# Kernel tuning notes

Measured on AMD Instinct MI355X. Metric: run time of the kernel, lower is better.

Reference implementation:

```python
import jax, jax.numpy as jnp
import numpy as np

EPS = 1e-5
TOP_K = 2


def setup_inputs() -> dict:
    key = jax.random.key(0)
    ks = jax.random.split(key, 8)
    B, T, D, E, F = 4, 2048, 1024, 8, 4096
    s_in = 1.0 / np.sqrt(D)
    s_ff = 1.0 / np.sqrt(F)
    return {
        "hidden_states": jax.random.normal(ks[0], (B, T, D), jnp.float32),
        "input_tensor": jax.random.normal(ks[1], (B, T, D), jnp.float32),
        "gate_w": jax.random.normal(ks[2], (D, E), jnp.float32) * s_in,
        "gate_b": jnp.zeros((E,), jnp.float32),
        "w1": jax.random.normal(ks[3], (E, D, F), jnp.float32) * s_in,
        "b1": jnp.zeros((E, F), jnp.float32),
        "w2": jax.random.normal(ks[4], (E, F, D), jnp.float32) * s_ff,
        "b2": jnp.zeros((E, D), jnp.float32),
        "gamma": jnp.ones((D,), jnp.float32),
        "beta": jnp.zeros((D,), jnp.float32),
    }


def _layer_norm(x, gamma, beta):
    mu = jnp.mean(x, axis=-1, keepdims=True)
    var = jnp.mean(jnp.square(x - mu), axis=-1, keepdims=True)
    return (x - mu) * jax.lax.rsqrt(var + EPS) * gamma + beta


def reference(hidden_states, input_tensor, gate_w, gate_b, w1, b1, w2, b2, gamma, beta):
    E = gate_b.shape[0]
    # Router: softmax over experts, then top-k gate values/indices.
    gate_logits = jnp.einsum("btd,de->bte", hidden_states, gate_w) + gate_b
    gate_probs = jax.nn.softmax(gate_logits, axis=-1)
    topk_gates, topk_idx = jax.lax.top_k(gate_probs, TOP_K)  # [B,T,K]
    # Combine weights per expert: sum of top-k gate values routed to expert e.
    combine_w = jnp.sum(
        jax.nn.one_hot(topk_idx, E, dtype=hidden_states.dtype)
        * topk_gates[..., None],
        axis=-2,
    )  # [B,T,E]
    # Dispatch/combine: weighted sum of expert FFN outputs (loop over small fixed E).
    expert_outputs = jnp.zeros_like(hidden_states)
    for e in range(E):
        h = jax.nn.gelu(jnp.einsum("btd,df->btf", hidden_states, w1[e]) + b1[e])
        y = jnp.einsum("btf,fd->btd", h, w2[e]) + b2[e]
        expert_outputs = expert_outputs + combine_w[..., e:e + 1] * y
    # Dropout is identity in eval mode.
    return _layer_norm(expert_outputs + input_tensor, gamma, beta)
```

## Files before the change

kernel.cpp:

```cpp
#include <hip/hip_runtime.h>

#define TOKENS 8192
#define DIM 1024
#define NEXP 8
#define FDIM 4096

typedef __bf16 bf16x8 __attribute__((ext_vector_type(8)));
typedef float f32x4 __attribute__((ext_vector_type(4)));
typedef float f32x16 __attribute__((ext_vector_type(16)));

__device__ __forceinline__ unsigned short f2bf(float f) {
  unsigned u = __builtin_bit_cast(unsigned, f);
  u += 0x7fffu + ((u >> 16) & 1u);
  return (unsigned short)(u >> 16);
}

__device__ __forceinline__ float bf2f(unsigned short s) {
  unsigned u = (unsigned)s << 16;
  return __builtin_bit_cast(float, u);
}

__device__ __forceinline__ void gload16(const void* g, void* l) {
  __builtin_amdgcn_global_load_lds(
      (const __attribute__((address_space(1))) unsigned int*)g,
      (__attribute__((address_space(3))) unsigned int*)l, 16, 0, 0);
}

__global__ void zero_counts_kernel(int* counts) {
  if (threadIdx.x < NEXP) counts[threadIdx.x] = 0;
}

__global__ void scan_kernel(const int* counts, int* offs, int* nchk,
                            int* chunks0, int* chunks1) {
  if (threadIdx.x == 0) {
    int s = 0;
    for (int e = 0; e < NEXP; ++e) { offs[e] = s; s += counts[e]; }
    offs[NEXP] = s;
    int nc0 = 0, nc1 = 0;
    for (int e = 0; e < NEXP; ++e) {
      const int mt = (counts[e] + 127) >> 7;
      for (int mc = 0; mc < mt; mc += 4) {
        for (int n4 = 0; n4 < 32; n4 += 4)
          chunks0[nc0++] = (e << 16) | (mc << 8) | n4;
        for (int n4 = 0; n4 < 8; n4 += 4)
          chunks1[nc1++] = (e << 16) | (mc << 8) | n4;
      }
    }
    nchk[0] = nc0;
    nchk[1] = nc1;
  }
}

__global__ void router_kernel(const float* __restrict__ hs,
                              const float* __restrict__ gw,
                              const float* __restrict__ gb,
                              int* __restrict__ counts,
                              int* __restrict__ tok_idx,
                              float* __restrict__ tok_w,
                              unsigned int* __restrict__ slotinfo,
                              unsigned short* __restrict__ hs_bf) {
  const int lane = threadIdx.x & 63;
  const int wid = threadIdx.x >> 6;
  const int t = blockIdx.x * 4 + wid;
  const float* row = hs + (size_t)t * DIM;

  float x[16];
  const float4* r4 = (const float4*)(row + lane * 16);
#pragma unroll
  for (int i = 0; i < 4; ++i) {
    float4 v = r4[i];
    x[i * 4 + 0] = v.x; x[i * 4 + 1] = v.y; x[i * 4 + 2] = v.z; x[i * 4 + 3] = v.w;
  }

  float acc[8];
#pragma unroll
  for (int e = 0; e < 8; ++e) acc[e] = 0.f;
#pragma unroll
  for (int i = 0; i < 16; ++i) {
    const int d = lane * 16 + i;
    const float4* g4 = (const float4*)(gw + (size_t)d * 8);
    float4 g0 = g4[0], g1 = g4[1];
    const float xv = x[i];
    acc[0] += xv * g0.x; acc[1] += xv * g0.y; acc[2] += xv * g0.z; acc[3] += xv * g0.w;
    acc[4] += xv * g1.x; acc[5] += xv * g1.y; acc[6] += xv * g1.z; acc[7] += xv * g1.w;
  }
#pragma unroll
  for (int sh = 1; sh < 64; sh <<= 1) {
#pragma unroll
    for (int e = 0; e < 8; ++e) acc[e] += __shfl_xor(acc[e], sh, 64);
  }
#pragma unroll
  for (int e = 0; e < 8; ++e) acc[e] += gb[e];

  float mx = acc[0];
#pragma unroll
  for (int e = 1; e < 8; ++e) mx = fmaxf(mx, acc[e]);
  float p[8];
  float sum = 0.f;
#pragma unroll
  for (int e = 0; e < 8; ++e) { p[e] = __expf(acc[e] - mx); sum += p[e]; }
  const float inv = 1.0f / sum;

  int i0 = 0; float b0 = p[0];
#pragma unroll
  for (int e = 1; e < 8; ++e) if (p[e] > b0) { b0 = p[e]; i0 = e; }
  int i1 = -1; float b1v = -1.f;
#pragma unroll
  for (int e = 0; e < 8; ++e) if (e != i0 && p[e] > b1v) { b1v = p[e]; i1 = e; }

  if (lane == 0) {
    int pos0 = atomicAdd(&counts[i0], 1);
    tok_idx[i0 * TOKENS + pos0] = t;
    tok_w[i0 * TOKENS + pos0] = b0 * inv;
    int pos1 = atomicAdd(&counts[i1], 1);
    tok_idx[i1 * TOKENS + pos1] = t;
    tok_w[i1 * TOKENS + pos1] = b1v * inv;
    slotinfo[t] = ((unsigned)i0 << 29) | ((unsigned)pos0 << 16) |
                  ((unsigned)i1 << 13) | (unsigned)pos1;
  }

  unsigned short us[16];
#pragma unroll
  for (int i = 0; i < 16; ++i) us[i] = f2bf(x[i]);
  uint4 o0, o1;
  o0.x = (unsigned)us[0] | ((unsigned)us[1] << 16);
  o0.y = (unsigned)us[2] | ((unsigned)us[3] << 16);
  o0.z = (unsigned)us[4] | ((unsigned)us[5] << 16);
  o0.w = (unsigned)us[6] | ((unsigned)us[7] << 16);
  o1.x = (unsigned)us[8] | ((unsigned)us[9] << 16);
  o1.y = (unsigned)us[10] | ((unsigned)us[11] << 16);
  o1.z = (unsigned)us[12] | ((unsigned)us[13] << 16);
  o1.w = (unsigned)us[14] | ((unsigned)us[15] << 16);
  uint4* dst = (uint4*)(hs_bf + (size_t)t * DIM + lane * 16);
  dst[0] = o0;
  dst[1] = o1;
}

__global__ void cast_transpose_all(const float* __restrict__ w1,
                                   unsigned short* __restrict__ w1t,
                                   const float* __restrict__ w2,
                                   unsigned short* __restrict__ w2t) {
  __shared__ float tile[64][65];
  const int L = blockIdx.x;
  const float* src;
  unsigned short* dstp;
  int R, C, bi;
  if (L < 8192) { src = w1; dstp = w1t; R = DIM;  C = FDIM; bi = L; }
  else          { src = w2; dstp = w2t; R = FDIM; C = DIM;  bi = L - 8192; }
  const int nx = C >> 6;
  const int e = bi >> 10;
  const int w = bi & 1023;
  const int by = w / nx, bx = w % nx;
  const int r0 = by * 64, c0 = bx * 64;
  const float* s = src + (size_t)e * R * C;
  unsigned int* d = (unsigned int*)(dstp + (size_t)e * R * C);

#pragma unroll
  for (int i = 0; i < 16; ++i) {
    const int idx = threadIdx.x + i * 256;
    const int r = idx >> 6;
    const int c = idx & 63;
    tile[r][c] = s[(size_t)(r0 + r) * C + (c0 + c)];
  }
  __syncthreads();
#pragma unroll
  for (int i = 0; i < 8; ++i) {
    const int idx = threadIdx.x + i * 256;
    const int c = idx >> 5;
    const int r = (idx & 31) * 2;
    unsigned pk = (unsigned)f2bf(tile[r][c]) | ((unsigned)f2bf(tile[r + 1][c]) << 16);
    d[((size_t)(c0 + c) * R + (r0 + r)) >> 1] = pk;
  }
}

template<int MODE, int K, int N>
__global__ __launch_bounds__(256, 4)
void moe_gemm(const unsigned short* __restrict__ Abase,
              const unsigned short* __restrict__ Bbase,
              const float* __restrict__ bias,
              const int* __restrict__ counts,
              const int* __restrict__ offs,
              const int* __restrict__ tok_idx,
              const int* __restrict__ chunktab,
              const int* __restrict__ nchk,
              unsigned short* __restrict__ dst) {
  constexpr int NS = K / 32;
  __shared__ __align__(16) unsigned char sm[32768];

  const int L = blockIdx.x;
  const int xk = L & 7;
  const int tt = L >> 3;
  const int g = (tt >> 4) * 8 + xk;
  if (g >= nchk[MODE]) return;
  const int within = tt & 15;
  const int cd = chunktab[g];
  const int e = cd >> 16;
  const int cnt = counts[e];
  const int m0 = (((cd >> 8) & 255) + (within >> 2)) * 128;
  if (m0 >= cnt) return;
  const int n0 = ((cd & 255) + (within & 3)) * 128;
  const int goff = offs[e];

  const int tid = threadIdx.x;
  const int lane = tid & 63;
  const int wid = tid >> 6;
  const int wm = wid >> 1;
  const int wn = wid & 1;
  const int l31 = lane & 31;
  const int lh = lane >> 5;

  const int trow = tid >> 2;
  const int tswz = (tid & 3) ^ ((trow >> 1) & 3);
  const unsigned char* Bexp = (const unsigned char*)(Bbase + (size_t)e * K * N);

  int gA0 = m0 + trow;      if (gA0 > cnt - 1) gA0 = cnt - 1;
  int gA1 = m0 + trow + 64; if (gA1 > cnt - 1) gA1 = cnt - 1;
  size_t rowA0, rowA1;
  if (MODE == 0) {
    rowA0 = (size_t)tok_idx[e * TOKENS + gA0] * K;
    rowA1 = (size_t)tok_idx[e * TOKENS + gA1] * K;
  } else {
    rowA0 = (size_t)(goff + gA0) * K;
    rowA1 = (size_t)(goff + gA1) * K;
  }
  const unsigned char* pA0 = (const unsigned char*)(Abase + rowA0) + tswz * 16;
  const unsigned char* pA1 = (const unsigned char*)(Abase + rowA1) + tswz * 16;
  const unsigned char* pB0 = Bexp + (size_t)(n0 + trow) * (K * 2) + tswz * 16;
  const unsigned char* pB1 = Bexp + (size_t)(n0 + trow + 64) * (K * 2) + tswz * 16;

  const int sw = (l31 >> 1) & 3;
  const int cE = lh ^ sw;
  const int aB = wm * 4096 + l31 * 64 + cE * 16;
  const int bB = 8192 + wn * 4096 + l31 * 64 + cE * 16;
  const unsigned char* smc = (const unsigned char*)sm;
  unsigned char* smw = (unsigned char*)sm + tid * 16;

  f32x16 acc[2][2];
#pragma unroll
  for (int mb = 0; mb < 2; ++mb)
#pragma unroll
    for (int nb = 0; nb < 2; ++nb)
#pragma unroll
      for (int r = 0; r < 16; ++r) acc[mb][nb][r] = 0.f;

  gload16(pA0, smw);
  gload16(pA1, smw + 4096);
  gload16(pB0, smw + 8192);
  gload16(pB1, smw + 12288);
  pA0 += 64; pA1 += 64; pB0 += 64; pB1 += 64;

#pragma unroll 1
  for (int st = 0; st < NS; ++st) {
    const int cs = (st & 1) << 14;
    const int ns = ((st + 1) & 1) << 14;
    if (st < NS - 1) {
      gload16(pA0, smw + ns);
      gload16(pA1, smw + ns + 4096);
      gload16(pB0, smw + ns + 8192);
      gload16(pB1, smw + ns + 12288);
      pA0 += 64; pA1 += 64; pB0 += 64; pB1 += 64;
      asm volatile("s_waitcnt vmcnt(4)" ::: "memory");
    } else {
      asm volatile("s_waitcnt vmcnt(0)" ::: "memory");
    }
    __builtin_amdgcn_s_barrier();
    __builtin_amdgcn_sched_barrier(0);
#pragma unroll
    for (int kq = 0; kq < 2; ++kq) {
      const int ko = kq << 5;
      bf16x8 a0 = *(const bf16x8*)(smc + cs + (aB ^ ko));
      bf16x8 a1 = *(const bf16x8*)(smc + cs + ((aB + 2048) ^ ko));
      bf16x8 b0 = *(const bf16x8*)(smc + cs + (bB ^ ko));
      bf16x8 b1 = *(const bf16x8*)(smc + cs + ((bB + 2048) ^ ko));
      acc[0][0] = __builtin_amdgcn_mfma_f32_32x32x16_bf16(a0, b0, acc[0][0], 0, 0, 0);
      acc[0][1] = __builtin_amdgcn_mfma_f32_32x32x16_bf16(a0, b1, acc[0][1], 0, 0, 0);
      acc[1][0] = __builtin_amdgcn_mfma_f32_32x32x16_bf16(a1, b0, acc[1][0], 0, 0, 0);
      acc[1][1] = __builtin_amdgcn_mfma_f32_32x32x16_bf16(a1, b1, acc[1][1], 0, 0, 0);
    }
    __builtin_amdgcn_sched_barrier(0);
    asm volatile("s_waitcnt lgkmcnt(0)" ::: "memory");
    __builtin_amdgcn_s_barrier();
  }

#pragma unroll
  for (int nb = 0; nb < 2; ++nb) {
    const int fcol = n0 + wn * 64 + nb * 32 + l31;
    const float bv = bias[e * N + fcol];
#pragma unroll
    for (int mb = 0; mb < 2; ++mb) {
#pragma unroll
      for (int r = 0; r < 16; ++r) {
        const int ml = wm * 64 + mb * 32 + (r & 3) + 8 * (r >> 2) + 4 * lh;
        const int gm = m0 + ml;
        if (gm < cnt) {
          float v = acc[mb][nb][r] + bv;
          if (MODE == 0) {
            const float u = 0.7978845608028654f * (v + 0.044715f * v * v * v);
            const float th = 1.0f - 2.0f / (1.0f + __expf(2.0f * u));
            v = 0.5f * v * (1.0f + th);
          }
          dst[(size_t)(goff + gm) * N + fcol] = f2bf(v);
        }
      }
    }
  }
}

__global__ void ln_combine_kernel(const unsigned short* __restrict__ y_buf,
                                  const float* __restrict__ in_t,
                                  const int* __restrict__ offs,
                                  const unsigned int* __restrict__ slotinfo,
                                  const float* __restrict__ tok_w,
                                  const float* __restrict__ gamma,
                                  const float* __restrict__ beta,
                                  float* __restrict__ out) {
  const int lane = threadIdx.x & 63;
  const int wid = threadIdx.x >> 6;
  const int t = blockIdx.x * 4 + wid;

  const unsigned s = slotinfo[t];
  const int e0 = s >> 29, p0 = (s >> 16) & 8191;
  const int e1 = (s >> 13) & 7, p1 = s & 8191;
  const float w0 = tok_w[e0 * TOKENS + p0];
  const float w1 = tok_w[e1 * TOKENS + p1];
  const size_t r0 = (size_t)(offs[e0] + p0) * DIM;
  const size_t r1 = (size_t)(offs[e1] + p1) * DIM;

  float v[16];
  {
    const float4* i4 = (const float4*)(in_t + (size_t)t * DIM + lane * 16);
    const uint4* y0 = (const uint4*)(y_buf + r0 + lane * 16);
    const uint4* y1 = (const uint4*)(y_buf + r1 + lane * 16);
#pragma unroll
    for (int i = 0; i < 4; ++i) {
      float4 a = i4[i];
      v[i * 4 + 0] = a.x; v[i * 4 + 1] = a.y; v[i * 4 + 2] = a.z; v[i * 4 + 3] = a.w;
    }
#pragma unroll
    for (int i = 0; i < 2; ++i) {
      uint4 u0 = y0[i];
      uint4 u1 = y1[i];
      const unsigned uw0[4] = {u0.x, u0.y, u0.z, u0.w};
      const unsigned uw1[4] = {u1.x, u1.y, u1.z, u1.w};
#pragma unroll
      for (int k = 0; k < 4; ++k) {
        const int base = i * 8 + k * 2;
        v[base + 0] += w0 * bf2f((unsigned short)(uw0[k] & 0xffff)) +
                       w1 * bf2f((unsigned short)(uw1[k] & 0xffff));
        v[base + 1] += w0 * bf2f((unsigned short)(uw0[k] >> 16)) +
                       w1 * bf2f((unsigned short)(uw1[k] >> 16));
      }
    }
  }

  float sum = 0.f, s2 = 0.f;
#pragma unroll
  for (int i = 0; i < 16; ++i) { sum += v[i]; s2 += v[i] * v[i]; }
#pragma unroll
  for (int sh = 1; sh < 64; sh <<= 1) {
    sum += __shfl_xor(sum, sh, 64);
    s2 += __shfl_xor(s2, sh, 64);
  }
  const float mu = sum * (1.0f / DIM);
  const float var = s2 * (1.0f / DIM) - mu * mu;
  const float rs = rsqrtf(var + 1e-5f);

  float4* w4 = (float4*)(out + (size_t)t * DIM + lane * 16);
#pragma unroll
  for (int i = 0; i < 4; ++i) {
    const int d = lane * 16 + i * 4;
    float4 gg = *(const float4*)(gamma + d);
    float4 bb = *(const float4*)(beta + d);
    float4 o;
    o.x = (v[i * 4 + 0] - mu) * rs * gg.x + bb.x;
    o.y = (v[i * 4 + 1] - mu) * rs * gg.y + bb.y;
    o.z = (v[i * 4 + 2] - mu) * rs * gg.z + bb.z;
    o.w = (v[i * 4 + 3] - mu) * rs * gg.w + bb.w;
    w4[i] = o;
  }
}

extern "C" void kernel_launch(void* const* d_in, const int* in_sizes, int n_in,
                              void* d_out, int out_size, void* d_ws, size_t ws_size,
                              hipStream_t stream) {
  const float* hs    = (const float*)d_in[0];
  const float* in_t  = (const float*)d_in[1];
  const float* gw    = (const float*)d_in[2];
  const float* gb    = (const float*)d_in[3];
  const float* w1    = (const float*)d_in[4];
  const float* b1    = (const float*)d_in[5];
  const float* w2    = (const float*)d_in[6];
  const float* b2    = (const float*)d_in[7];
  const float* gamma = (const float*)d_in[8];
  const float* beta  = (const float*)d_in[9];
  float* out = (float*)d_out;
  char* ws = (char*)d_ws;

  int* counts            = (int*)(ws + 0);
  int* offs              = (int*)(ws + 256);
  unsigned int* slotinfo = (unsigned int*)(ws + 512);
  int* nchk              = (int*)(ws + 33280);
  int* chunks0           = (int*)(ws + 33536);
  int* chunks1           = (int*)(ws + 35072);
  int* tok_idx           = (int*)(ws + 66048);
  float* tok_w           = (float*)(ws + 328192);
  unsigned short* hs_bf  = (unsigned short*)(ws + 590336);
  unsigned short* w1t    = (unsigned short*)(ws + 17367552);
  unsigned short* w2t    = (unsigned short*)(ws + 84476416);
  unsigned short* h_buf  = (unsigned short*)(ws + 151585280);
  unsigned short* y_buf  = (unsigned short*)(ws + 590336);

  zero_counts_kernel<<<1, 64, 0, stream>>>(counts);
  router_kernel<<<TOKENS / 4, 256, 0, stream>>>(hs, gw, gb, counts, tok_idx, tok_w,
                                                slotinfo, hs_bf);
  scan_kernel<<<1, 64, 0, stream>>>(counts, offs, nchk, chunks0, chunks1);
  cast_transpose_all<<<16384, 256, 0, stream>>>(w1, w1t, w2, w2t);
  moe_gemm<0, DIM, FDIM><<<6144, 256, 0, stream>>>(
      hs_bf, w1t, b1, counts, offs, tok_idx, chunks0, nchk, h_buf);
  moe_gemm<1, FDIM, DIM><<<2048, 256, 0, stream>>>(
      h_buf, w2t, b2, counts, offs, tok_idx, chunks1, nchk, y_buf);
  ln_combine_kernel<<<TOKENS / 4, 256, 0, stream>>>(y_buf, in_t, offs, slotinfo,
                                                    tok_w, gamma, beta, out);
}
```

Baseline: 729.9 us.

## Drop zero and scan kernels, derive offsets inline, vectorize transpose loads, extend LDS swizzle

Removes the zero_counts and scan launches. Counts are now zeroed inside cast_transpose_all, which is moved ahead of the router, and each GEMM block and combine thread rebuilds its expert and chunk mapping and prefix offsets from counts itself. The weight cast-transpose reads float4 instead of scalars, and the LDS swizzle in the GEMM gains an extra XOR term to cut bank conflicts. The cost is a little redundant per-block scan work, and correctness depends on the zeroing block finishing before the router's atomics, which stream ordering provides.

```diff
diff --git a/kernel.cpp b/kernel.cpp
--- a/kernel.cpp
+++ b/kernel.cpp
@@ -24,31 +24,6 @@
   __builtin_amdgcn_global_load_lds(
       (const __attribute__((address_space(1))) unsigned int*)g,
       (__attribute__((address_space(3))) unsigned int*)l, 16, 0, 0);
-}
-
-__global__ void zero_counts_kernel(int* counts) {
-  if (threadIdx.x < NEXP) counts[threadIdx.x] = 0;
-}
-
-__global__ void scan_kernel(const int* counts, int* offs, int* nchk,
-                            int* chunks0, int* chunks1) {
-  if (threadIdx.x == 0) {
-    int s = 0;
-    for (int e = 0; e < NEXP; ++e) { offs[e] = s; s += counts[e]; }
-    offs[NEXP] = s;
-    int nc0 = 0, nc1 = 0;
-    for (int e = 0; e < NEXP; ++e) {
-      const int mt = (counts[e] + 127) >> 7;
-      for (int mc = 0; mc < mt; mc += 4) {
-        for (int n4 = 0; n4 < 32; n4 += 4)
-          chunks0[nc0++] = (e << 16) | (mc << 8) | n4;
-        for (int n4 = 0; n4 < 8; n4 += 4)
-          chunks1[nc1++] = (e << 16) | (mc << 8) | n4;
-      }
-    }
-    nchk[0] = nc0;
-    nchk[1] = nc1;
-  }
 }
 
 __global__ void router_kernel(const float* __restrict__ hs,
@@ -139,9 +114,11 @@
 __global__ void cast_transpose_all(const float* __restrict__ w1,
                                    unsigned short* __restrict__ w1t,
                                    const float* __restrict__ w2,
-                                   unsigned short* __restrict__ w2t) {
+                                   unsigned short* __restrict__ w2t,
+                                   int* __restrict__ counts) {
   __shared__ float tile[64][65];
   const int L = blockIdx.x;
+  if (L == 0 && threadIdx.x < NEXP) counts[threadIdx.x] = 0;
   const float* src;
   unsigned short* dstp;
   int R, C, bi;
@@ -156,11 +133,13 @@
   unsigned int* d = (unsigned int*)(dstp + (size_t)e * R * C);
 
 #pragma unroll
-  for (int i = 0; i < 16; ++i) {
+  for (int i = 0; i < 4; ++i) {
     const int idx = threadIdx.x + i * 256;
-    const int r = idx >> 6;
-    const int c = idx & 63;
-    tile[r][c] = s[(size_t)(r0 + r) * C + (c0 + c)];
+    const int r = idx >> 4;
+    const int c4 = (idx & 15) * 4;
+    float4 v = *(const float4*)(s + (size_t)(r0 + r) * C + (c0 + c4));
+    tile[r][c4 + 0] = v.x; tile[r][c4 + 1] = v.y;
+    tile[r][c4 + 2] = v.z; tile[r][c4 + 3] = v.w;
   }
   __syncthreads();
 #pragma unroll
@@ -179,27 +158,45 @@
               const unsigned short* __restrict__ Bbase,
               const float* __restrict__ bias,
               const int* __restrict__ counts,
-              const int* __restrict__ offs,
               const int* __restrict__ tok_idx,
-              const int* __restrict__ chunktab,
-              const int* __restrict__ nchk,
               unsigned short* __restrict__ dst) {
   constexpr int NS = K / 32;
+  constexpr int NQ = (MODE == 0) ? 8 : 2;
   __shared__ __align__(16) unsigned char sm[32768];
 
   const int L = blockIdx.x;
   const int xk = L & 7;
   const int tt = L >> 3;
   const int g = (tt >> 4) * 8 + xk;
-  if (g >= nchk[MODE]) return;
   const int within = tt & 15;
-  const int cd = chunktab[g];
-  const int e = cd >> 16;
-  const int cnt = counts[e];
-  const int m0 = (((cd >> 8) & 255) + (within >> 2)) * 128;
+
+  int e = 0, mcq = 0, n4 = 0, goff = 0, cnt = 0;
+  {
+    int accC = 0, accOff = 0;
+    bool found = false;
+#pragma unroll
+    for (int ee = 0; ee < NEXP; ++ee) {
+      const int c = counts[ee];
+      const int mt = (c + 127) >> 7;
+      const int mc4 = (mt + 3) >> 2;
+      const int ch = mc4 * NQ;
+      if (!found && g < accC + ch) {
+        const int local = g - accC;
+        e = ee;
+        mcq = (local / NQ) * 4;
+        n4 = (local % NQ) * 4;
+        goff = accOff;
+        cnt = c;
+        found = true;
+      }
+      accC += ch;
+      accOff += c;
+    }
+    if (!found) return;
+  }
+  const int m0 = (mcq + (within >> 2)) * 128;
   if (m0 >= cnt) return;
-  const int n0 = ((cd & 255) + (within & 3)) * 128;
-  const int goff = offs[e];
+  const int n0 = (n4 + (within & 3)) * 128;
 
   const int tid = threadIdx.x;
   const int lane = tid & 63;
@@ -210,7 +207,7 @@
   const int lh = lane >> 5;
 
   const int trow = tid >> 2;
-  const int tswz = (tid & 3) ^ ((trow >> 1) & 3);
+  const int tswz = (tid & 3) ^ ((trow >> 1) & 3) ^ ((trow >> 3) & 3);
   const unsigned char* Bexp = (const unsigned char*)(Bbase + (size_t)e * K * N);
 
   int gA0 = m0 + trow;      if (gA0 > cnt - 1) gA0 = cnt - 1;
@@ -228,7 +225,7 @@
   const unsigned char* pB0 = Bexp + (size_t)(n0 + trow) * (K * 2) + tswz * 16;
   const unsigned char* pB1 = Bexp + (size_t)(n0 + trow + 64) * (K * 2) + tswz * 16;
 
-  const int sw = (l31 >> 1) & 3;
+  const int sw = ((l31 >> 1) & 3) ^ ((l31 >> 3) & 3);
   const int cE = lh ^ sw;
   const int aB = wm * 4096 + l31 * 64 + cE * 16;
   const int bB = 8192 + wn * 4096 + l31 * 64 + cE * 16;
@@ -308,7 +305,7 @@
 
 __global__ void ln_combine_kernel(const unsigned short* __restrict__ y_buf,
                                   const float* __restrict__ in_t,
-                                  const int* __restrict__ offs,
+                                  const int* __restrict__ counts,
                                   const unsigned int* __restrict__ slotinfo,
                                   const float* __restrict__ tok_w,
                                   const float* __restrict__ gamma,
@@ -321,10 +318,17 @@
   const unsigned s = slotinfo[t];
   const int e0 = s >> 29, p0 = (s >> 16) & 8191;
   const int e1 = (s >> 13) & 7, p1 = s & 8191;
+  int off0 = 0, off1 = 0;
+#pragma unroll
+  for (int ee = 0; ee < NEXP; ++ee) {
+    const int c = counts[ee];
+    if (ee < e0) off0 += c;
+    if (ee < e1) off1 += c;
+  }
   const float w0 = tok_w[e0 * TOKENS + p0];
   const float w1 = tok_w[e1 * TOKENS + p1];
-  const size_t r0 = (size_t)(offs[e0] + p0) * DIM;
-  const size_t r1 = (size_t)(offs[e1] + p1) * DIM;
+  const size_t r0 = (size_t)(off0 + p0) * DIM;
+  const size_t r1 = (size_t)(off1 + p1) * DIM;
 
   float v[16];
   {
@@ -397,11 +401,7 @@
   char* ws = (char*)d_ws;
 
   int* counts            = (int*)(ws + 0);
-  int* offs              = (int*)(ws + 256);
   unsigned int* slotinfo = (unsigned int*)(ws + 512);
-  int* nchk              = (int*)(ws + 33280);
-  int* chunks0           = (int*)(ws + 33536);
-  int* chunks1           = (int*)(ws + 35072);
   int* tok_idx           = (int*)(ws + 66048);
   float* tok_w           = (float*)(ws + 328192);
   unsigned short* hs_bf  = (unsigned short*)(ws + 590336);
@@ -410,15 +410,13 @@
   unsigned short* h_buf  = (unsigned short*)(ws + 151585280);
   unsigned short* y_buf  = (unsigned short*)(ws + 590336);
 
-  zero_counts_kernel<<<1, 64, 0, stream>>>(counts);
+  cast_transpose_all<<<16384, 256, 0, stream>>>(w1, w1t, w2, w2t, counts);
   router_kernel<<<TOKENS / 4, 256, 0, stream>>>(hs, gw, gb, counts, tok_idx, tok_w,
                                                 slotinfo, hs_bf);
-  scan_kernel<<<1, 64, 0, stream>>>(counts, offs, nchk, chunks0, chunks1);
-  cast_transpose_all<<<16384, 256, 0, stream>>>(w1, w1t, w2, w2t);
   moe_gemm<0, DIM, FDIM><<<6144, 256, 0, stream>>>(
-      hs_bf, w1t, b1, counts, offs, tok_idx, chunks0, nchk, h_buf);
+      hs_bf, w1t, b1, counts, tok_idx, h_buf);
   moe_gemm<1, FDIM, DIM><<<2048, 256, 0, stream>>>(
-      h_buf, w2t, b2, counts, offs, tok_idx, chunks1, nchk, y_buf);
-  ln_combine_kernel<<<TOKENS / 4, 256, 0, stream>>>(y_buf, in_t, offs, slotinfo,
+      h_buf, w2t, b2, counts, tok_idx, y_buf);
+  ln_combine_kernel<<<TOKENS / 4, 256, 0, stream>>>(y_buf, in_t, counts, slotinfo,
                                                     tok_w, gamma, beta, out);
 }
```

New measurement: 715.2 us. 1.02x faster.
